# Kernel optimization log

Hardware: AMD Instinct MI355X
Metric: run time of the kernel (lower is better)

The kernel has to match this reference:

```python
import jax, jax.numpy as jnp
import numpy as np

ROW_DIMS = (8, 10, 20, 20)   # factorization of vocab = 32000
COL_DIMS = (4, 4, 6, 8)      # factorization of out_features = 768
RANKS = (1, 16, 16, 16, 1)
VOCAB = int(np.prod(ROW_DIMS))
OUT = int(np.prod(COL_DIMS))
# cum_prod[k] = prod(ROW_DIMS[k+1:]) -> mixed-radix digit extraction
CUM_PROD = np.concatenate([np.cumprod(ROW_DIMS[::-1])[::-1][1:], [1]]).astype(np.int32)


def setup_inputs() -> dict:
    key = jax.random.key(0)
    ks = jax.random.split(key, 5)
    x = jax.random.randint(ks[0], (8, 4096), 0, VOCAB, dtype=jnp.int32)
    cores = {}
    for k in range(4):
        shp = (RANKS[k], ROW_DIMS[k], COL_DIMS[k], RANKS[k + 1])
        # scale so that the product of 4 cores has ~unit stddev per element
        std = 1.0 / np.sqrt(RANKS[k + 1])
        cores[f"core{k}"] = (jax.random.normal(ks[k + 1], shp, dtype=jnp.float32) * std)
    return {"x": x, **cores}


def reference(x, core0, core1, core2, core3):
    cores = (core0, core1, core2, core3)
    idx = x.reshape(-1)                 # [B] flattened token indices
    B = idx.shape[0]
    digits = [(idx // CUM_PROD[k]) % ROW_DIMS[k] for k in range(4)]
    # first core: [1, n0, m0, r1] -> gather -> [B, m0, r1]
    res = core0[0][digits[0]].reshape(B, COL_DIMS[0], RANKS[1])
    for k in range(1, 4):
        g = jnp.take(cores[k], digits[k], axis=1)        # [r_k, B, m_k, r_{k+1}]
        res = jnp.einsum('bar,rbms->bams', res, g)       # chain contraction over rank
        res = res.reshape(B, -1, RANKS[k + 1])
    rows = res.reshape(B, OUT)
    return rows.reshape(*x.shape, OUT)
```

## Files before the change

### kernel.cpp

```cpp
#include <hip/hip_runtime.h>


#define NTOK 32768
#define TPW  8
#define G2F_BYTES (400 * 3 * 64 * 16)
#define G1F_BYTES (80 * 64 * 16)
#define TBL_BYTES (G2F_BYTES + G1F_BYTES)

typedef _Float16 f16x8 __attribute__((ext_vector_type(8)));
typedef float f32x4 __attribute__((ext_vector_type(4)));

__device__ inline unsigned pack2(float x, float y) {
    _Float16 hx = (_Float16)x, hy = (_Float16)y;
    unsigned short ux = __builtin_bit_cast(unsigned short, hx);
    unsigned short uy = __builtin_bit_cast(unsigned short, hy);
    return (unsigned)ux | ((unsigned)uy << 16);
}

__global__ __launch_bounds__(256) void build_frag_tables(const float* __restrict__ core0,
                                                         const float* __restrict__ core1,
                                                         const float* __restrict__ core2,
                                                         const float* __restrict__ core3,
                                                         unsigned* __restrict__ g2f,
                                                         unsigned* __restrict__ g1f) {
    __shared__ float lds[768];
    int b = blockIdx.x, t = threadIdx.x;
    if (b < 400) {
        int d2 = b / 20, d3 = b % 20;
#pragma unroll
        for (int i = 0; i < 3; ++i) {
            int f = t + i * 256;
            int r2 = f / 48, mc = f - r2 * 48;
            int m2 = mc >> 3, m3 = mc & 7;
            float acc = 0.f;
#pragma unroll
            for (int r3 = 0; r3 < 16; ++r3)
                acc += core2[((r2 * 20 + d2) * 6 + m2) * 16 + r3] *
                       core3[(r3 * 20 + d3) * 8 + m3];
            lds[f] = acc;
        }
        __syncthreads();
        int l = t >> 2, jp = t & 3;
        int k0 = ((l >> 4) << 3) + jp * 2;
        int mcl = l & 15;
        bool valid = k0 < 16;
#pragma unroll
        for (int p = 0; p < 3; ++p) {
            int mc = p * 16 + mcl;
            float v0 = valid ? lds[k0 * 48 + mc] : 0.f;
            float v1 = valid ? lds[(k0 + 1) * 48 + mc] : 0.f;
            g2f[(b * 3 + p) * 256 + t] = pack2(v0, v1);
        }
    } else {
        int combo = b - 400;
        int d0 = combo / 10, d1 = combo % 10;
        int a = t >> 4, r2 = t & 15;
        int a0 = a >> 2, m1 = a & 3;
        float acc = 0.f;
#pragma unroll
        for (int r1 = 0; r1 < 16; ++r1)
            acc += core0[(d0 * 4 + a0) * 16 + r1] *
                   core1[((r1 * 10 + d1) * 4 + m1) * 16 + r2];
        lds[t] = acc;
        __syncthreads();
        int l = t >> 2, jp = t & 3;
        int k0 = ((l >> 4) << 3) + jp * 2;
        int al = l & 15;
        bool valid = k0 < 16;
        float v0 = valid ? lds[al * 16 + k0] : 0.f;
        float v1 = valid ? lds[al * 16 + k0 + 1] : 0.f;
        g1f[combo * 256 + t] = pack2(v0, v1);
    }
}

__global__ __launch_bounds__(256) void te_mfma(const int* __restrict__ x,
                                               const f16x8* __restrict__ g2f,
                                               const f16x8* __restrict__ g1f,
                                               float* __restrict__ out) {
    const int wave = threadIdx.x >> 6, lane = threadIdx.x & 63;
    const int tok0 = (blockIdx.x * 4 + wave) * TPW;

    int4 xa = ((const int4*)(x + tok0))[0];
    int4 xb = ((const int4*)(x + tok0))[1];
    int idxs[TPW] = {xa.x, xa.y, xa.z, xa.w, xb.x, xb.y, xb.z, xb.w};

    f16x8 A0, A1, A2, B;
    {
        int id = idxs[0];
        const f16x8* ap = g2f + (size_t)(id % 400) * 192 + lane;
        A0 = ap[0]; A1 = ap[64]; A2 = ap[128];
        B = g1f[(id / 400) * 64 + lane];
    }
    const f32x4 z = {0.f, 0.f, 0.f, 0.f};
    float* obase = out + (size_t)tok0 * 768 + (lane & 15) * 48 + ((lane >> 4) << 2);

#pragma unroll
    for (int t = 0; t < TPW; ++t) {
        int tn = (t + 1 < TPW) ? t + 1 : t;
        int id = idxs[tn];
        const f16x8* ap = g2f + (size_t)(id % 400) * 192 + lane;
        f16x8 nA0 = ap[0], nA1 = ap[64], nA2 = ap[128];
        f16x8 nB = g1f[(id / 400) * 64 + lane];

        f32x4 d0 = __builtin_amdgcn_mfma_f32_16x16x32_f16(A0, B, z, 0, 0, 0);
        f32x4 d1 = __builtin_amdgcn_mfma_f32_16x16x32_f16(A1, B, z, 0, 0, 0);
        f32x4 d2 = __builtin_amdgcn_mfma_f32_16x16x32_f16(A2, B, z, 0, 0, 0);

        float* o = obase + t * 768;
        *(f32x4*)(o)      = d0;
        *(f32x4*)(o + 16) = d1;
        *(f32x4*)(o + 32) = d2;

        A0 = nA0; A1 = nA1; A2 = nA2; B = nB;
    }
}

__global__ void te_direct(const int* __restrict__ x,
                          const float* __restrict__ core0,
                          const float* __restrict__ core1,
                          const float* __restrict__ core2,
                          const float* __restrict__ core3,
                          float* __restrict__ out) {
    int tok = blockIdx.x;
    int lane = threadIdx.x;
    int idx = x[tok];
    int d0 = idx / 4000;
    int rem = idx - d0 * 4000;
    int d1 = rem / 400;
    rem -= d1 * 400;
    int d2 = rem / 20;
    int d3 = rem - d2 * 20;
    float* o = out + (size_t)tok * 768;
    for (int p = 0; p < 3; ++p) {
        int base = (p * 64 + lane) * 4;
        int a = base / 48;
        int mc = base - a * 48;
        int a0 = a >> 2, m1 = a & 3;
        float s[16];
#pragma unroll
        for (int r2 = 0; r2 < 16; ++r2) {
            float acc = 0.f;
            for (int r1 = 0; r1 < 16; ++r1)
                acc += core0[(d0 * 4 + a0) * 16 + r1] *
                       core1[((r1 * 10 + d1) * 4 + m1) * 16 + r2];
            s[r2] = acc;
        }
        float4 accv = {0.f, 0.f, 0.f, 0.f};
        float* accp = (float*)&accv;
        for (int j = 0; j < 4; ++j) {
            int mcj = mc + j;
            int m2 = mcj >> 3, m3 = mcj & 7;
            float tt = 0.f;
            for (int r2 = 0; r2 < 16; ++r2) {
                float g = 0.f;
                for (int r3 = 0; r3 < 16; ++r3)
                    g += core2[((r2 * 20 + d2) * 6 + m2) * 16 + r3] *
                         core3[(r3 * 20 + d3) * 8 + m3];
                tt += s[r2] * g;
            }
            accp[j] = tt;
        }
        *(float4*)(o + base) = accv;
    }
}

extern "C" void kernel_launch(void* const* d_in, const int* in_sizes, int n_in,
                              void* d_out, int out_size, void* d_ws, size_t ws_size,
                              hipStream_t stream) {
    const int*   x     = (const int*)d_in[0];
    const float* core0 = (const float*)d_in[1];
    const float* core1 = (const float*)d_in[2];
    const float* core2 = (const float*)d_in[3];
    const float* core3 = (const float*)d_in[4];
    float* out = (float*)d_out;

    if (ws_size >= (size_t)TBL_BYTES) {
        unsigned* g2f = (unsigned*)d_ws;
        unsigned* g1f = (unsigned*)((char*)d_ws + G2F_BYTES);
        build_frag_tables<<<480, 256, 0, stream>>>(core0, core1, core2, core3,
                                                   g2f, g1f);
        te_mfma<<<NTOK / (4 * TPW), 256, 0, stream>>>(x, (const f16x8*)g2f,
                                                      (const f16x8*)g1f, out);
    } else {
        te_direct<<<NTOK, 64, 0, stream>>>(x, core0, core1, core2, core3, out);
    }
}
```

Measured before the change: 29.67 us.

## Use K=16 MFMA with compact fragment tables and two-deep prefetch

Switches from the 16x16x32 MFMA, which padded half of K with zeros, to the 16x16x16 variant. The fragment tables shrink to match: A is stored as one 8-wide fragment plus one 4-wide fragment, and B as a 4-wide fragment. This halves the gather traffic per token from the tables. Prefetch depth grows from one to two tokens to hide gather latency, at the cost of more live registers.

```diff
diff --git a/kernel.cpp b/kernel.cpp
--- a/kernel.cpp
+++ b/kernel.cpp
@@ -3,10 +3,13 @@
 
 #define NTOK 32768
 #define TPW  8
-#define G2F_BYTES (400 * 3 * 64 * 16)
-#define G1F_BYTES (80 * 64 * 16)
-#define TBL_BYTES (G2F_BYTES + G1F_BYTES)
-
+#define NBLK (NTOK / (4 * TPW))
+#define G2A01_BYTES (400 * 64 * 16)
+#define G2A2_BYTES  (400 * 64 * 8)
+#define G1B_BYTES   (80 * 64 * 8)
+#define TBL_BYTES   (G2A01_BYTES + G2A2_BYTES + G1B_BYTES)
+
+typedef _Float16 f16x4 __attribute__((ext_vector_type(4)));
 typedef _Float16 f16x8 __attribute__((ext_vector_type(8)));
 typedef float f32x4 __attribute__((ext_vector_type(4)));
 
@@ -21,10 +24,12 @@
                                                          const float* __restrict__ core1,
                                                          const float* __restrict__ core2,
                                                          const float* __restrict__ core3,
-                                                         unsigned* __restrict__ g2f,
-                                                         unsigned* __restrict__ g1f) {
+                                                         unsigned* __restrict__ g2a01,
+                                                         unsigned* __restrict__ g2a2,
+                                                         unsigned* __restrict__ g1b) {
     __shared__ float lds[768];
     int b = blockIdx.x, t = threadIdx.x;
+    int l = t & 63, part = t >> 6;
     if (b < 400) {
         int d2 = b / 20, d3 = b % 20;
 #pragma unroll
@@ -40,16 +45,19 @@
             lds[f] = acc;
         }
         __syncthreads();
-        int l = t >> 2, jp = t & 3;
-        int k0 = ((l >> 4) << 3) + jp * 2;
-        int mcl = l & 15;
-        bool valid = k0 < 16;
-#pragma unroll
-        for (int p = 0; p < 3; ++p) {
-            int mc = p * 16 + mcl;
-            float v0 = valid ? lds[k0 * 48 + mc] : 0.f;
-            float v1 = valid ? lds[(k0 + 1) * 48 + mc] : 0.f;
-            g2f[(b * 3 + p) * 256 + t] = pack2(v0, v1);
+        {
+            int pp = part >> 1;
+            int jp = part & 1;
+            int k = ((l >> 4) << 2) + jp * 2;
+            int mc = pp * 16 + (l & 15);
+            g2a01[(b * 64 + l) * 4 + part] = pack2(lds[k * 48 + mc],
+                                                   lds[(k + 1) * 48 + mc]);
+        }
+        if (part < 2) {
+            int k = ((l >> 4) << 2) + part * 2;
+            int mc = 32 + (l & 15);
+            g2a2[(b * 64 + l) * 2 + part] = pack2(lds[k * 48 + mc],
+                                                  lds[(k + 1) * 48 + mc]);
         }
     } else {
         int combo = b - 400;
@@ -63,19 +71,33 @@
                    core1[((r1 * 10 + d1) * 4 + m1) * 16 + r2];
         lds[t] = acc;
         __syncthreads();
-        int l = t >> 2, jp = t & 3;
-        int k0 = ((l >> 4) << 3) + jp * 2;
-        int al = l & 15;
-        bool valid = k0 < 16;
-        float v0 = valid ? lds[al * 16 + k0] : 0.f;
-        float v1 = valid ? lds[al * 16 + k0 + 1] : 0.f;
-        g1f[combo * 256 + t] = pack2(v0, v1);
-    }
+        if (part < 2) {
+            int k = ((l >> 4) << 2) + part * 2;
+            int n = l & 15;
+            g1b[(combo * 64 + l) * 2 + part] = pack2(lds[n * 16 + k],
+                                                     lds[n * 16 + k + 1]);
+        }
+    }
+}
+
+struct Frag { f16x8 a01; f16x4 a2; f16x4 b; };
+
+__device__ inline Frag load_frag(int id, int lane,
+                                 const f16x8* __restrict__ g2a01,
+                                 const f16x4* __restrict__ g2a2,
+                                 const f16x4* __restrict__ g1b) {
+    Frag f;
+    int c23 = id % 400, c01 = id / 400;
+    f.a01 = g2a01[c23 * 64 + lane];
+    f.a2  = g2a2[c23 * 64 + lane];
+    f.b   = g1b[c01 * 64 + lane];
+    return f;
 }
 
 __global__ __launch_bounds__(256) void te_mfma(const int* __restrict__ x,
-                                               const f16x8* __restrict__ g2f,
-                                               const f16x8* __restrict__ g1f,
+                                               const f16x8* __restrict__ g2a01,
+                                               const f16x4* __restrict__ g2a2,
+                                               const f16x4* __restrict__ g1b,
                                                float* __restrict__ out) {
     const int wave = threadIdx.x >> 6, lane = threadIdx.x & 63;
     const int tok0 = (blockIdx.x * 4 + wave) * TPW;
@@ -84,34 +106,30 @@
     int4 xb = ((const int4*)(x + tok0))[1];
     int idxs[TPW] = {xa.x, xa.y, xa.z, xa.w, xb.x, xb.y, xb.z, xb.w};
 
-    f16x8 A0, A1, A2, B;
-    {
-        int id = idxs[0];
-        const f16x8* ap = g2f + (size_t)(id % 400) * 192 + lane;
-        A0 = ap[0]; A1 = ap[64]; A2 = ap[128];
-        B = g1f[(id / 400) * 64 + lane];
-    }
+    Frag f0 = load_frag(idxs[0], lane, g2a01, g2a2, g1b);
+    Frag f1 = load_frag(idxs[1], lane, g2a01, g2a2, g1b);
+
     const f32x4 z = {0.f, 0.f, 0.f, 0.f};
     float* obase = out + (size_t)tok0 * 768 + (lane & 15) * 48 + ((lane >> 4) << 2);
 
 #pragma unroll
     for (int t = 0; t < TPW; ++t) {
-        int tn = (t + 1 < TPW) ? t + 1 : t;
-        int id = idxs[tn];
-        const f16x8* ap = g2f + (size_t)(id % 400) * 192 + lane;
-        f16x8 nA0 = ap[0], nA1 = ap[64], nA2 = ap[128];
-        f16x8 nB = g1f[(id / 400) * 64 + lane];
-
-        f32x4 d0 = __builtin_amdgcn_mfma_f32_16x16x32_f16(A0, B, z, 0, 0, 0);
-        f32x4 d1 = __builtin_amdgcn_mfma_f32_16x16x32_f16(A1, B, z, 0, 0, 0);
-        f32x4 d2 = __builtin_amdgcn_mfma_f32_16x16x32_f16(A2, B, z, 0, 0, 0);
+        Frag f2 = f1;
+        if (t + 2 < TPW)
+            f2 = load_frag(idxs[t + 2], lane, g2a01, g2a2, g1b);
+
+        f16x4 a0 = __builtin_shufflevector(f0.a01, f0.a01, 0, 1, 2, 3);
+        f16x4 a1 = __builtin_shufflevector(f0.a01, f0.a01, 4, 5, 6, 7);
+        f32x4 d0 = __builtin_amdgcn_mfma_f32_16x16x16f16(a0,    f0.b, z, 0, 0, 0);
+        f32x4 d1 = __builtin_amdgcn_mfma_f32_16x16x16f16(a1,    f0.b, z, 0, 0, 0);
+        f32x4 d2 = __builtin_amdgcn_mfma_f32_16x16x16f16(f0.a2, f0.b, z, 0, 0, 0);
 
         float* o = obase + t * 768;
         *(f32x4*)(o)      = d0;
         *(f32x4*)(o + 16) = d1;
         *(f32x4*)(o + 32) = d2;
 
-        A0 = nA0; A1 = nA1; A2 = nA2; B = nB;
+        f0 = f1; f1 = f2;
     }
 }
 
@@ -175,12 +193,14 @@
     float* out = (float*)d_out;
 
     if (ws_size >= (size_t)TBL_BYTES) {
-        unsigned* g2f = (unsigned*)d_ws;
-        unsigned* g1f = (unsigned*)((char*)d_ws + G2F_BYTES);
+        unsigned* g2a01 = (unsigned*)d_ws;
+        unsigned* g2a2  = (unsigned*)((char*)d_ws + G2A01_BYTES);
+        unsigned* g1b   = (unsigned*)((char*)d_ws + G2A01_BYTES + G2A2_BYTES);
         build_frag_tables<<<480, 256, 0, stream>>>(core0, core1, core2, core3,
-                                                   g2f, g1f);
-        te_mfma<<<NTOK / (4 * TPW), 256, 0, stream>>>(x, (const f16x8*)g2f,
-                                                      (const f16x8*)g1f, out);
+                                                   g2a01, g2a2, g1b);
+        te_mfma<<<NBLK, 256, 0, stream>>>(x, (const f16x8*)g2a01,
+                                          (const f16x4*)g2a2,
+                                          (const f16x4*)g1b, out);
     } else {
         te_direct<<<NTOK, 64, 0, stream>>>(x, core0, core1, core2, core3, out);
     }
```

Measured after the change: 27.66 us. 1.07x faster.
